# Optimization experiments

Hardware: AMD Instinct MI355X
Metric: run time of the kernel (lower is better)

The kernel has to match this reference:

```python
import jax, jax.numpy as jnp
import numpy as np

N, T, C = 2048, 32, 512          # stocks, lookback, channels (= embed_dim)
H, DH = 8, 64                    # heads, head_dim
NUM_IND = 64                     # number of industries
K1, S1, TS1 = 2, 2, 16           # conv scale 1
K2, S2, TS2 = 4, 4, 8            # conv scale 2
TC = T + TS1 + TS2               # concat_time_dim_for_triu = 56
EPS = 1e-5


def hardswish(x):
    return x * jnp.clip(x + 3.0, 0.0, 6.0) / 6.0


def _conv1d(x_nct, w, b, stride):
    # x_nct: [N, C, T], w: [C_out, C_in, K]
    y = jax.lax.conv_general_dilated(x_nct, w, (stride,), 'VALID',
                                     dimension_numbers=('NCH', 'OIH', 'NCH'))
    return y + b[None, :, None]


def _ln2d(y, g, b):
    # torch LayerNorm([ts, C]): normalize jointly over last two dims
    m = y.mean(axis=(-2, -1), keepdims=True)
    v = y.var(axis=(-2, -1), keepdims=True)
    return (y - m) / jnp.sqrt(v + EPS) * g + b


def _time_mixer(x, conv1_w, conv1_b, conv2_w, conv2_b,
                ln1_g, ln1_b, ln2_g, ln2_b,
                triu_w1, triu_b1, triu_w2, triu_b2):
    x_nct = x.transpose(0, 2, 1)                                   # [N, C, T]
    f1 = _ln2d(_conv1d(x_nct, conv1_w, conv1_b, S1).transpose(0, 2, 1), ln1_g, ln1_b)  # [N, TS1, C]
    f2 = _ln2d(_conv1d(x_nct, conv2_w, conv2_b, S2).transpose(0, 2, 1), ln2_g, ln2_b)  # [N, TS2, C]
    cat = jnp.concatenate([x, f1, f2], axis=1)                     # [N, TC, C]
    z = cat.transpose(0, 2, 1)                                     # [N, C, TC]
    # TriU: per-timestep Linear(i+1 -> 1) == lower-triangular matmul + bias
    h = jnp.einsum('nct,st->ncs', z, jnp.tril(triu_w1)) + triu_b1
    h = hardswish(h)
    h = jnp.einsum('nct,st->ncs', h, jnp.tril(triu_w2)) + triu_b2
    return h.transpose(0, 2, 1)                                    # [N, TC, C]


def _sparse_attn(tokens, industry_ids, wq, bq, wk, bk, wv, bv, wo, bo):
    # tokens: [N, C]; same-industry block-sparse attention (eval: no dropout)
    q = (tokens @ wq + bq).reshape(N, H, DH)
    k = (tokens @ wk + bk).reshape(N, H, DH)
    v = (tokens @ wv + bv).reshape(N, H, DH)
    scores = jnp.einsum('nhd,mhd->hnm', q, k) / jnp.sqrt(jnp.float32(DH))  # [H, N, N]
    mask = industry_ids[:, None] == industry_ids[None, :]                  # [N, N]
    scores = jnp.where(mask[None], scores, jnp.float32(-1e9))
    attn = jax.nn.softmax(scores, axis=-1)
    out = jnp.einsum('hnm,mhd->nhd', attn, v).reshape(N, C)
    return out @ wo + bo


def setup_inputs() -> dict:
    key = jax.random.key(0)
    ks = jax.random.split(key, 20)
    g = lambda k, s, sc=0.02: jax.random.normal(k, s, jnp.float32) * sc
    return {
        'x': jax.random.normal(ks[0], (N, T, C), jnp.float32),
        'industry_ids': jax.random.randint(ks[1], (N,), 0, NUM_IND),
        'conv1_w': g(ks[2], (C, C, K1)), 'conv1_b': jnp.zeros((C,), jnp.float32),
        'conv2_w': g(ks[3], (C, C, K2)), 'conv2_b': jnp.zeros((C,), jnp.float32),
        'ln1_g': jnp.ones((TS1, C), jnp.float32), 'ln1_b': jnp.zeros((TS1, C), jnp.float32),
        'ln2_g': jnp.ones((TS2, C), jnp.float32), 'ln2_b': jnp.zeros((TS2, C), jnp.float32),
        'triu_w1': g(ks[4], (TC, TC), 0.1), 'triu_b1': jnp.zeros((TC,), jnp.float32),
        'triu_w2': g(ks[5], (TC, TC), 0.1), 'triu_b2': jnp.zeros((TC,), jnp.float32),
        'wq': g(ks[6], (C, C)), 'bq': jnp.zeros((C,), jnp.float32),
        'wk': g(ks[7], (C, C)), 'bk': jnp.zeros((C,), jnp.float32),
        'wv': g(ks[8], (C, C)), 'bv': jnp.zeros((C,), jnp.float32),
        'wo': g(ks[9], (C, C)), 'bo': jnp.zeros((C,), jnp.float32),
        'wp': g(ks[10], (C, 1)), 'bp': jnp.zeros((1,), jnp.float32),
    }


def reference(x, industry_ids, conv1_w, conv1_b, conv2_w, conv2_b,
              ln1_g, ln1_b, ln2_g, ln2_b,
              triu_w1, triu_b1, triu_w2, triu_b2,
              wq, bq, wk, bk, wv, bv, wo, bo, wp, bp):
    mixed = _time_mixer(x, conv1_w, conv1_b, conv2_w, conv2_b,
                        ln1_g, ln1_b, ln2_g, ln2_b,
                        triu_w1, triu_b1, triu_w2, triu_b2)   # [N, TC, C]
    pooled = mixed.mean(axis=1)                                # [N, C]
    attn = _sparse_attn(pooled, industry_ids, wq, bq, wk, bk, wv, bv, wo, bo)
    h = pooled + attn                                          # residual
    return h @ wp + bp                                         # [N, 1]
```

## Files before the change

kernel.cpp:

```cpp
#include <hip/hip_runtime.h>

#define NST 2048

typedef __attribute__((ext_vector_type(8))) short bf16x8;
typedef __attribute__((ext_vector_type(4))) float f32x4;
typedef __attribute__((ext_vector_type(8))) unsigned short u16x8;

__device__ __forceinline__ float hswish(float x) {
  return x * fminf(fmaxf(x + 3.f, 0.f), 6.f) * (1.f / 6.f);
}

__device__ __forceinline__ unsigned short f2bf(float f) {
  unsigned int u = __float_as_uint(f);
  u += 0x7fffu + ((u >> 16) & 1u);
  return (unsigned short)(u >> 16);
}

__device__ __forceinline__ float bf2f(unsigned short b) {
  return __uint_as_float(((unsigned int)b) << 16);
}

__device__ __forceinline__ void gload16(const void* g, void* l) {
  __builtin_amdgcn_global_load_lds(
      (const __attribute__((address_space(1))) void*)g,
      (__attribute__((address_space(3))) void*)l, 16, 0, 0);
}

__global__ __launch_bounds__(256) void x_prep(const float* __restrict__ x,
                                              unsigned short* __restrict__ xbf,
                                              unsigned short* __restrict__ xT) {
  __shared__ unsigned short T[32 * 520];
  const int n = blockIdx.x;
  const int tid = threadIdx.x;
  const float* xn = x + (long)n * 16384;
  unsigned short* xbn = xbf + (long)n * 16384;

#pragma unroll
  for (int i = 0; i < 16; i++) {
    int id = tid + i * 256;
    int flat = id * 4;
    float4 v = *(const float4*)(xn + flat);
    short4 o;
    o.x = (short)f2bf(v.x); o.y = (short)f2bf(v.y);
    o.z = (short)f2bf(v.z); o.w = (short)f2bf(v.w);
    *(short4*)(xbn + flat) = o;
    int t = flat >> 9, c = flat & 511;
    *(short4*)&T[t * 520 + c] = o;
  }
  __syncthreads();

#pragma unroll
  for (int r = 0; r < 2; r++) {
    int c = tid + r * 256;
    unsigned short* dst = xT + ((long)n * 512 + c) * 32;
#pragma unroll
    for (int q = 0; q < 4; q++) {
      short4 o;
      o.x = (short)T[(q * 8 + 0) * 520 + c];
      o.y = (short)T[(q * 8 + 1) * 520 + c];
      o.z = (short)T[(q * 8 + 2) * 520 + c];
      o.w = (short)T[(q * 8 + 3) * 520 + c];
      short4 p;
      p.x = (short)T[(q * 8 + 4) * 520 + c];
      p.y = (short)T[(q * 8 + 5) * 520 + c];
      p.z = (short)T[(q * 8 + 6) * 520 + c];
      p.w = (short)T[(q * 8 + 7) * 520 + c];
      *(short4*)(dst + q * 8) = o;
      *(short4*)(dst + q * 8 + 4) = p;
    }
  }
}

__global__ __launch_bounds__(256) void conv_w_to_bt(const float* __restrict__ src,
                                                    unsigned short* __restrict__ dst,
                                                    int Kw, int rlshift) {
  int id = blockIdx.x * 256 + threadIdx.x;
  int co = id >> rlshift;
  int idx = id & ((1 << rlshift) - 1);
  int ci = idx & 511;
  int k = idx >> 9;
  dst[id] = f2bf(src[((co << 9) + ci) * Kw + k]);
}

__global__ __launch_bounds__(256) void qkv_w_to_bt(
    const float* __restrict__ wq, const float* __restrict__ wk,
    const float* __restrict__ wv, const float* __restrict__ bq,
    const float* __restrict__ bk, const float* __restrict__ bv,
    unsigned short* __restrict__ Bt, float* __restrict__ bias) {
  int id = blockIdx.x * 256 + threadIdx.x;
  int o = id >> 9, i = id & 511;
  int oc = o & 511;
  const float* w = (o < 512) ? wq : (o < 1024) ? wk : wv;
  Bt[id] = f2bf(w[(i << 9) + oc]);
  if (i == 0) bias[o] = (o < 512) ? bq[oc] : (o < 1024) ? bk[oc] : bv[oc];
}

__global__ __launch_bounds__(256) void triu_prep(
    const float* __restrict__ W1, const float* __restrict__ b1,
    const float* __restrict__ W2, const float* __restrict__ b2,
    unsigned short* __restrict__ W1bf, float* __restrict__ w2cp,
    float* __restrict__ b1p, float* __restrict__ b2s) {
  int tid = threadIdx.x;
#pragma unroll
  for (int i = 0; i < 16; i++) {
    int id = tid + i * 256;
    int s = id >> 6, t = id & 63;
    float v = (s < 56 && t < 56 && t <= s) ? W1[s * 56 + t] : 0.f;
    W1bf[id] = f2bf(v);
  }
  if (tid < 64) {
    float sum = 0.f;
    if (tid < 56)
      for (int r = tid; r < 56; r++) sum += W2[r * 56 + tid];
    w2cp[tid] = sum;
    b1p[tid] = (tid < 56) ? b1[tid] : 0.f;
  }
  if (tid == 0) {
    float b = 0.f;
    for (int s = 0; s < 56; s++) b += b2[s];
    b2s[0] = b;
  }
}

template <int MODE>
__global__ __launch_bounds__(256) void gemm_bt(
    const unsigned short* __restrict__ A, const unsigned short* __restrict__ Bt,
    float* __restrict__ C, unsigned short* __restrict__ fT,
    const float* __restrict__ bias, int K, int ldc) {
  __shared__ unsigned short As[128 * 64];
  __shared__ unsigned short Bs[128 * 64];
  const int tid = threadIdx.x;
  const int wid = tid >> 6;
  const int lane = tid & 63;
  const int r0 = blockIdx.x * 128;
  const int c0 = blockIdx.y * 128;
  const int wr = (wid >> 1) * 64;
  const int wc = (wid & 1) * 64;
  const int srow = lane >> 3;
  const int sslot = lane & 7;

  long aoffl[4], boffl[4];
  unsigned short* adst[4];
  unsigned short* bdst[4];
#pragma unroll
  for (int l = 0; l < 4; l++) {
    const int r = (wid * 4 + l) * 8 + srow;
    const int gr = r0 + r;
    long ao;
    if (MODE == 0)      ao = (long)(((gr >> 4) * 32) + ((gr & 15) << 1)) << 9;
    else if (MODE == 1) ao = (long)(((gr >> 3) * 32) + ((gr & 7) << 2)) << 9;
    else                ao = (long)gr * K;
    const int sw = (sslot ^ (r & 7)) << 3;
    aoffl[l] = ao + sw;
    boffl[l] = (long)(c0 + r) * K + sw;
    adst[l] = &As[(wid * 4 + l) * 8 * 64];
    bdst[l] = &Bs[(wid * 4 + l) * 8 * 64];
  }

  f32x4 acc[4][4];
#pragma unroll
  for (int m = 0; m < 4; m++)
#pragma unroll
    for (int n = 0; n < 4; n++) acc[m][n] = (f32x4){0.f, 0.f, 0.f, 0.f};

  const int fr = lane & 15;
  const int fq = lane >> 4;

  for (int kt = 0; kt < K; kt += 64) {
#pragma unroll
    for (int l = 0; l < 4; l++) {
      gload16(A + aoffl[l] + kt, adst[l]);
      gload16(Bt + boffl[l] + kt, bdst[l]);
    }
    __syncthreads();
#pragma unroll
    for (int ks = 0; ks < 2; ks++) {
      const int kq = ks * 4 + fq;
      bf16x8 af[4], bfr[4];
#pragma unroll
      for (int m = 0; m < 4; m++) {
        const int rr = wr + m * 16 + fr;
        af[m] = *(const bf16x8*)&As[rr * 64 + ((kq ^ (rr & 7)) << 3)];
      }
#pragma unroll
      for (int n = 0; n < 4; n++) {
        const int cc = wc + n * 16 + fr;
        bfr[n] = *(const bf16x8*)&Bs[cc * 64 + ((kq ^ (cc & 7)) << 3)];
      }
#pragma unroll
      for (int m = 0; m < 4; m++)
#pragma unroll
        for (int n = 0; n < 4; n++)
          acc[m][n] = __builtin_amdgcn_mfma_f32_16x16x32_bf16(
              af[m], bfr[n], acc[m][n], 0, 0, 0);
    }
    __syncthreads();
  }

  float bv[4];
#pragma unroll
  for (int n = 0; n < 4; n++) bv[n] = bias[c0 + wc + n * 16 + fr];

  if (MODE == 2) {
#pragma unroll
    for (int m = 0; m < 4; m++)
#pragma unroll
      for (int j = 0; j < 4; j++) {
        const int gr = r0 + wr + m * 16 + fq * 4 + j;
        float* cp = C + (long)gr * ldc + c0 + wc + fr;
#pragma unroll
        for (int n = 0; n < 4; n++) cp[n * 16] = acc[m][n][j] + bv[n];
      }
  } else {
#pragma unroll
    for (int m = 0; m < 4; m++) {
      const int gr = r0 + wr + m * 16 + fq * 4;
      int nst, e0;
      if (MODE == 0) { nst = gr >> 4; e0 = gr & 15; }
      else           { nst = gr >> 3; e0 = 16 + (gr & 7); }
#pragma unroll
      for (int n = 0; n < 4; n++) {
        const int cc = c0 + wc + n * 16 + fr;
        short4 o;
        o.x = (short)f2bf(acc[m][n][0] + bv[n]);
        o.y = (short)f2bf(acc[m][n][1] + bv[n]);
        o.z = (short)f2bf(acc[m][n][2] + bv[n]);
        o.w = (short)f2bf(acc[m][n][3] + bv[n]);
        *(short4*)(fT + ((long)(nst * 512 + cc) * 32 + e0)) = o;
      }
    }
  }
}

__global__ __launch_bounds__(256) void ln_fT(
    unsigned short* __restrict__ fT,
    const float* __restrict__ g1, const float* __restrict__ b1,
    const float* __restrict__ g2, const float* __restrict__ b2) {
  const int n = blockIdx.x;
  const int tid = threadIdx.x;
  const int w = tid >> 6, lane = tid & 63;
  __shared__ float red[4][4];
  unsigned short* base = fT + (long)n * 16384;

  u16x8 ch[8];
  float s1 = 0.f, q1 = 0.f, s2 = 0.f, q2 = 0.f;
#pragma unroll
  for (int i = 0; i < 8; i++) {
    int id = tid + i * 256;
    int qq = id & 3;
    if (qq != 3) {
      u16x8 v = *(const u16x8*)(base + (long)id * 8);
      ch[i] = v;
      float fs = 0.f, fq = 0.f;
#pragma unroll
      for (int j = 0; j < 8; j++) {
        float f = bf2f(v[j]);
        fs += f; fq += f * f;
      }
      if (qq < 2) { s1 += fs; q1 += fq; } else { s2 += fs; q2 += fq; }
    }
  }
  for (int d = 32; d; d >>= 1) {
    s1 += __shfl_down(s1, d); q1 += __shfl_down(q1, d);
    s2 += __shfl_down(s2, d); q2 += __shfl_down(q2, d);
  }
  if (lane == 0) { red[w][0] = s1; red[w][1] = q1; red[w][2] = s2; red[w][3] = q2; }
  __syncthreads();
  float S1 = red[0][0] + red[1][0] + red[2][0] + red[3][0];
  float Q1 = red[0][1] + red[1][1] + red[2][1] + red[3][1];
  float S2 = red[0][2] + red[1][2] + red[2][2] + red[3][2];
  float Q2 = red[0][3] + red[1][3] + red[2][3] + red[3][3];
  float m1 = S1 / 8192.f, v1 = Q1 / 8192.f - m1 * m1;
  float r1 = rsqrtf(v1 + 1e-5f);
  float m2 = S2 / 4096.f, v2 = Q2 / 4096.f - m2 * m2;
  float r2 = rsqrtf(v2 + 1e-5f);

#pragma unroll
  for (int i = 0; i < 8; i++) {
    int id = tid + i * 256;
    int qq = id & 3, c = id >> 2;
    u16x8 o;
    if (qq == 3) {
#pragma unroll
      for (int j = 0; j < 8; j++) o[j] = 0;
    } else {
      float m = (qq < 2) ? m1 : m2;
      float r = (qq < 2) ? r1 : r2;
#pragma unroll
      for (int j = 0; j < 8; j++) {
        float g, b;
        if (qq < 2) { int ts = qq * 8 + j; g = g1[ts * 512 + c]; b = b1[ts * 512 + c]; }
        else        { g = g2[j * 512 + c]; b = b2[j * 512 + c]; }
        float f = bf2f(ch[i][j]);
        o[j] = f2bf((f - m) * r * g + b);
      }
    }
    *(u16x8*)(base + (long)id * 8) = o;
  }
}

__global__ __launch_bounds__(512, 4) void triu_pool(
    const unsigned short* __restrict__ xT, const unsigned short* __restrict__ fT,
    const unsigned short* __restrict__ W1bf, const float* __restrict__ b1p,
    const float* __restrict__ w2cp, const float* __restrict__ b2s,
    float* __restrict__ pooled, unsigned short* __restrict__ pooledbf) {
  __shared__ unsigned short Zt[512 * 64];
  const int tid = threadIdx.x;
  const int wid = tid >> 6;
  const int lane = tid & 63;
  const int n = blockIdx.x;
  const int fr = lane & 15;
  const int fq = lane >> 4;

  const unsigned short* xTn = xT + (long)n * 16384;
  const unsigned short* fTn = fT + (long)n * 16384;

#pragma unroll
  for (int cb = 0; cb < 8; cb++) {
    const int cbase = wid * 64 + cb * 8;
    const int c = cbase + (lane >> 3);
    const int slot = lane & 7;
    const int slotp = slot ^ (c & 7);
    const unsigned short* src = (slotp < 4)
        ? (xTn + c * 32 + slotp * 8)
        : (fTn + c * 32 + (slotp - 4) * 8);
    gload16(src, &Zt[cbase * 64]);
  }
  __syncthreads();

  bf16x8 afr[4][2];
#pragma unroll
  for (int m = 0; m < 4; m++)
#pragma unroll
    for (int ks = 0; ks < 2; ks++)
      afr[m][ks] = *(const bf16x8*)(W1bf + (m * 16 + fr) * 64 + ks * 32 + fq * 8);

  f32x4 acc[4][4];
#pragma unroll
  for (int m = 0; m < 4; m++)
#pragma unroll
    for (int nn = 0; nn < 4; nn++) acc[m][nn] = (f32x4){0.f, 0.f, 0.f, 0.f};

#pragma unroll
  for (int nn = 0; nn < 4; nn++) {
    const int c = wid * 64 + nn * 16 + fr;
#pragma unroll
    for (int ks = 0; ks < 2; ks++) {
      const int slot = (ks * 4 + fq) ^ (c & 7);
      bf16x8 bfrag = *(const bf16x8*)&Zt[c * 64 + slot * 8];
#pragma unroll
      for (int m = 0; m < 4; m++)
        acc[m][nn] = __builtin_amdgcn_mfma_f32_16x16x32_bf16(
            afr[m][ks], bfrag, acc[m][nn], 0, 0, 0);
    }
  }

  float b1r[16], w2r[16];
#pragma unroll
  for (int m = 0; m < 4; m++)
#pragma unroll
    for (int j = 0; j < 4; j++) {
      int s = m * 16 + fq * 4 + j;
      b1r[m * 4 + j] = b1p[s];
      w2r[m * 4 + j] = w2cp[s];
    }
  const float b2sum = b2s[0];

#pragma unroll
  for (int nn = 0; nn < 4; nn++) {
    float cs = 0.f;
#pragma unroll
    for (int m = 0; m < 4; m++)
#pragma unroll
      for (int j = 0; j < 4; j++)
        cs = fmaf(hswish(acc[m][nn][j] + b1r[m * 4 + j]), w2r[m * 4 + j], cs);
    cs += __shfl_xor(cs, 16);
    cs += __shfl_xor(cs, 32);
    if (fq == 0) {
      const int c = wid * 64 + nn * 16 + fr;
      float pv = (cs + b2sum) * (1.f / 56.f);
      pooled[(long)n * 512 + c] = pv;
      pooledbf[(long)n * 512 + c] = f2bf(pv);
    }
  }
}

__global__ void binzero(int* counts, int* cursor) {
  int i = threadIdx.x;
  if (i < 64) { counts[i] = 0; cursor[i] = 0; }
}
__global__ void bincount(const int* __restrict__ ids, int* counts) {
  int n = blockIdx.x * 256 + threadIdx.x;
  if (n < NST) atomicAdd(&counts[ids[n]], 1);
}
__global__ void binscan(const int* __restrict__ counts, int* offs) {
  int lane = threadIdx.x;
  int incl = counts[lane];
  for (int d = 1; d < 64; d <<= 1) {
    int u = __shfl_up(incl, d);
    if (lane >= d) incl += u;
  }
  offs[lane + 1] = incl;
  if (lane == 0) offs[0] = 0;
}
__global__ void binscatter(const int* __restrict__ ids, const int* __restrict__ offs,
                           int* cursor, int* perm) {
  int n = blockIdx.x * 256 + threadIdx.x;
  if (n < NST) {
    int g = ids[n];
    int pos = offs[g] + atomicAdd(&cursor[g], 1);
    perm[pos] = n;
  }
}

__global__ __launch_bounds__(256) void attn_kernel(
    const float* __restrict__ qkv, const int* __restrict__ offs,
    const int* __restrict__ perm, float* __restrict__ attnv) {
  const int g = blockIdx.x, h = blockIdx.y;
  const int off = offs[g];
  const int S = offs[g + 1] - off;
  const int tid = threadIdx.x;
  const int w = tid >> 6, lane = tid & 63;

  __shared__ float Ks[128 * 66];
  __shared__ float Vs[128 * 64];
  __shared__ float Ps[4][128];
  __shared__ float Qw[4][64];

  if (S <= 128) {
    for (int idx = tid; idx < S * 16; idx += 256) {
      const int row = idx >> 4, q4 = (idx & 15) * 4;
      const int mj = perm[off + row];
      const float* base = qkv + (long)mj * 1536 + h * 64 + q4;
      float4 kv = *(const float4*)(base + 512);
      float4 vv = *(const float4*)(base + 1024);
      float* kr = &Ks[row * 66 + q4];
      kr[0] = kv.x; kr[1] = kv.y; kr[2] = kv.z; kr[3] = kv.w;
      *(float4*)&Vs[row * 64 + q4] = vv;
    }
    __syncthreads();

    for (int i = w; i < S; i += 4) {
      const int mi = perm[off + i];
      const float qd = qkv[(long)mi * 1536 + h * 64 + lane];
      Qw[w][lane] = qd;

      float sc0 = -1e30f, sc1 = -1e30f;
      {
        const int j = lane;
        if (j < S) {
          float a = 0.f;
          const float* kr = &Ks[j * 66];
#pragma unroll
          for (int t = 0; t < 32; t++) {
            float2 k2 = *(const float2*)(kr + 2 * t);
            float2 q2 = *(const float2*)&Qw[w][2 * t];
            a = fmaf(q2.x, k2.x, a);
            a = fmaf(q2.y, k2.y, a);
          }
          sc0 = a * 0.125f;
        }
      }
      if (S > 64) {
        const int j = 64 + lane;
        if (j < S) {
          float a = 0.f;
          const float* kr = &Ks[j * 66];
#pragma unroll
          for (int t = 0; t < 32; t++) {
            float2 k2 = *(const float2*)(kr + 2 * t);
            float2 q2 = *(const float2*)&Qw[w][2 * t];
            a = fmaf(q2.x, k2.x, a);
            a = fmaf(q2.y, k2.y, a);
          }
          sc1 = a * 0.125f;
        }
      }
      float m = fmaxf(sc0, sc1);
      for (int d = 32; d; d >>= 1) m = fmaxf(m, __shfl_xor(m, d));
      float p0 = (lane < S) ? __expf(sc0 - m) : 0.f;
      float p1 = (64 + lane < S) ? __expf(sc1 - m) : 0.f;
      float l = p0 + p1;
      for (int d = 32; d; d >>= 1) l += __shfl_xor(l, d);
      Ps[w][lane] = p0;
      Ps[w][64 + lane] = p1;

      float o = 0.f;
      for (int j = 0; j < S; j++)
        o = fmaf(Ps[w][j], Vs[j * 64 + lane], o);
      attnv[(long)mi * 512 + h * 64 + lane] = o / l;
    }
  } else {
    __shared__ float pbuf[4][64];
    __shared__ int jbuf[4][64];
    for (int i = w; i < S; i += 4) {
      const int mi = perm[off + i];
      const float* qp = qkv + (long)mi * 1536 + h * 64;
      float m_run = -1e30f, l_run = 0.f, o_d = 0.f;
      for (int jb = 0; jb < S; jb += 64) {
        int jc = min(64, S - jb);
        int mj = (lane < jc) ? perm[off + jb + lane] : 0;
        float sc = -1e30f;
        if (lane < jc) {
          const float* kp = qkv + (long)mj * 1536 + 512 + h * 64;
          float a = 0.f;
#pragma unroll
          for (int d4 = 0; d4 < 16; d4++) {
            float4 qv = *(const float4*)(qp + d4 * 4);
            float4 kv = *(const float4*)(kp + d4 * 4);
            a += qv.x * kv.x + qv.y * kv.y + qv.z * kv.z + qv.w * kv.w;
          }
          sc = a * 0.125f;
        }
        float cm = sc;
        for (int d = 32; d; d >>= 1) cm = fmaxf(cm, __shfl_xor(cm, d));
        float m_new = fmaxf(m_run, cm);
        float resc = __expf(m_run - m_new);
        float p = (lane < jc) ? __expf(sc - m_new) : 0.f;
        float cs = p;
        for (int d = 32; d; d >>= 1) cs += __shfl_xor(cs, d);
        l_run = l_run * resc + cs;
        pbuf[w][lane] = p;
        jbuf[w][lane] = mj;
        float onew = o_d * resc;
        for (int j = 0; j < jc; j++)
          onew = fmaf(pbuf[w][j], qkv[(long)jbuf[w][j] * 1536 + 1024 + h * 64 + lane], onew);
        o_d = onew;
        m_run = m_new;
      }
      attnv[(long)mi * 512 + h * 64 + lane] = o_d / l_run;
    }
  }
}

__global__ void wowp_kernel(const float* __restrict__ wo, const float* __restrict__ wp,
                            const float* __restrict__ bo, const float* __restrict__ bp,
                            float* wowp, float* constbuf) {
  int w = threadIdx.x >> 6, lane = threadIdx.x & 63;
  int gw = blockIdx.x * 4 + w;
  for (int row = gw; row < 512; row += 32) {
    float partial = 0.f;
    for (int e = lane; e < 512; e += 64) partial += wo[(long)row * 512 + e] * wp[e];
    for (int d = 32; d; d >>= 1) partial += __shfl_xor(partial, d);
    if (lane == 0) wowp[row] = partial;
  }
  if (blockIdx.x == 0 && w == 0) {
    float partial = 0.f;
    for (int e = lane; e < 512; e += 64) partial += bo[e] * wp[e];
    for (int d = 32; d; d >>= 1) partial += __shfl_xor(partial, d);
    if (lane == 0) constbuf[0] = partial + bp[0];
  }
}

__global__ void final_kernel(const float* __restrict__ pooled,
                             const float* __restrict__ attnv,
                             const float* __restrict__ wp,
                             const float* __restrict__ wowp,
                             const float* __restrict__ constbuf,
                             float* __restrict__ out) {
  int w = threadIdx.x >> 6, lane = threadIdx.x & 63;
  int row = blockIdx.x * 4 + w;
  float partial = 0.f;
#pragma unroll
  for (int e8 = 0; e8 < 8; e8++) {
    int e = lane + e8 * 64;
    partial += pooled[(long)row * 512 + e] * wp[e] + attnv[(long)row * 512 + e] * wowp[e];
  }
  for (int d = 32; d; d >>= 1) partial += __shfl_xor(partial, d);
  if (lane == 0) out[row] = partial + constbuf[0];
}

extern "C" void kernel_launch(void* const* d_in, const int* in_sizes, int n_in,
                              void* d_out, int out_size, void* d_ws, size_t ws_size,
                              hipStream_t stream) {
  const float* x   = (const float*)d_in[0];
  const int*   ids = (const int*)d_in[1];
  const float* w1  = (const float*)d_in[2];
  const float* cb1 = (const float*)d_in[3];
  const float* w2  = (const float*)d_in[4];
  const float* cb2 = (const float*)d_in[5];
  const float* g1  = (const float*)d_in[6];
  const float* lb1 = (const float*)d_in[7];
  const float* g2  = (const float*)d_in[8];
  const float* lb2 = (const float*)d_in[9];
  const float* tw1 = (const float*)d_in[10];
  const float* tb1 = (const float*)d_in[11];
  const float* tw2 = (const float*)d_in[12];
  const float* tb2 = (const float*)d_in[13];
  const float* wq  = (const float*)d_in[14];
  const float* bq  = (const float*)d_in[15];
  const float* wk  = (const float*)d_in[16];
  const float* bk  = (const float*)d_in[17];
  const float* wv  = (const float*)d_in[18];
  const float* bv  = (const float*)d_in[19];
  const float* wo  = (const float*)d_in[20];
  const float* bo  = (const float*)d_in[21];
  const float* wp  = (const float*)d_in[22];
  const float* bp  = (const float*)d_in[23];
  float* out = (float*)d_out;

  char* ws = (char*)d_ws;
  size_t off = 0;
  auto alloc = [&](size_t bytes) {
    void* p = ws + off;
    off += (bytes + 255) & ~(size_t)255;
    return p;
  };
  unsigned short* xbf  = (unsigned short*)alloc((size_t)NST * 32 * 512 * 2);
  unsigned short* xT   = (unsigned short*)alloc((size_t)NST * 512 * 32 * 2);
  unsigned short* fT   = (unsigned short*)alloc((size_t)NST * 512 * 32 * 2);
  unsigned short* B1b  = (unsigned short*)alloc((size_t)512 * 1024 * 2);
  unsigned short* B2b  = (unsigned short*)alloc((size_t)512 * 2048 * 2);
  unsigned short* Bqkv = (unsigned short*)alloc((size_t)1536 * 512 * 2);
  float* bqkv   = (float*)alloc(1536 * 4);
  unsigned short* W1bf = (unsigned short*)alloc(64 * 64 * 2);
  float* w2cp   = (float*)alloc(64 * 4);
  float* b1p    = (float*)alloc(64 * 4);
  float* b2s    = (float*)alloc(4);
  float* pooled = (float*)alloc((size_t)NST * 512 * 4);
  unsigned short* pooledbf = (unsigned short*)alloc((size_t)NST * 512 * 2);
  float* qkvb   = (float*)alloc((size_t)NST * 1536 * 4);
  float* attnv  = (float*)alloc((size_t)NST * 512 * 4);
  float* wowp   = (float*)alloc(512 * 4);
  float* cbuf   = (float*)alloc(4);
  int* counts   = (int*)alloc(64 * 4);
  int* cursor   = (int*)alloc(64 * 4);
  int* offs     = (int*)alloc(65 * 4);
  int* perm     = (int*)alloc(NST * 4);

  x_prep<<<NST, 256, 0, stream>>>(x, xbf, xT);
  conv_w_to_bt<<<dim3(512 * 1024 / 256), 256, 0, stream>>>(w1, B1b, 2, 10);
  conv_w_to_bt<<<dim3(512 * 2048 / 256), 256, 0, stream>>>(w2, B2b, 4, 11);
  qkv_w_to_bt<<<dim3(1536 * 512 / 256), 256, 0, stream>>>(wq, wk, wv, bq, bk, bv, Bqkv, bqkv);
  triu_prep<<<1, 256, 0, stream>>>(tw1, tb1, tw2, tb2, W1bf, w2cp, b1p, b2s);
  binzero<<<1, 64, 0, stream>>>(counts, cursor);
  bincount<<<8, 256, 0, stream>>>(ids, counts);
  binscan<<<1, 64, 0, stream>>>(counts, offs);
  binscatter<<<8, 256, 0, stream>>>(ids, offs, cursor, perm);
  wowp_kernel<<<8, 256, 0, stream>>>(wo, wp, bo, bp, wowp, cbuf);

  gemm_bt<0><<<dim3(256, 4), 256, 0, stream>>>(xbf, B1b, nullptr, fT, cb1, 1024, 0);
  gemm_bt<1><<<dim3(128, 4), 256, 0, stream>>>(xbf, B2b, nullptr, fT, cb2, 2048, 0);
  ln_fT<<<NST, 256, 0, stream>>>(fT, g1, lb1, g2, lb2);
  triu_pool<<<NST, 512, 0, stream>>>(xT, fT, W1bf, b1p, w2cp, b2s, pooled, pooledbf);

  gemm_bt<2><<<dim3(16, 12), 256, 0, stream>>>(pooledbf, Bqkv, qkvb, nullptr, bqkv, 512, 1536);

  attn_kernel<<<dim3(64, 8), 256, 0, stream>>>(qkvb, offs, perm, attnv);
  final_kernel<<<512, 256, 0, stream>>>(pooled, attnv, wp, wowp, cbuf, out);
}
```

Measured before the change: 606.8 us.

## Merge prep kernels, fuse conv GEMMs, fold LayerNorm into triu_pool

Combines the weight-conversion, triu-prep and wo·wp kernels into a single launch, and collapses the four binning kernels into one block that uses shared-memory atomics. The two conv GEMMs become one grid, and the separate LayerNorm pass over fT is moved into triu_pool, which now normalises the data already staged in LDS. x_prep's transpose now uses 16-byte stores with a changed LDS padding. These changes remove several launches and one full read/write round trip of fT, at the cost of extra LDS work and a sync inside triu_pool.

```diff
diff --git a/kernel.cpp b/kernel.cpp
--- a/kernel.cpp
+++ b/kernel.cpp
@@ -29,7 +29,7 @@
 __global__ __launch_bounds__(256) void x_prep(const float* __restrict__ x,
                                               unsigned short* __restrict__ xbf,
                                               unsigned short* __restrict__ xT) {
-  __shared__ unsigned short T[32 * 520];
+  __shared__ unsigned short T[32 * 524];
   const int n = blockIdx.x;
   const int tid = threadIdx.x;
   const float* xn = x + (long)n * 16384;
@@ -45,88 +45,219 @@
     o.z = (short)f2bf(v.z); o.w = (short)f2bf(v.w);
     *(short4*)(xbn + flat) = o;
     int t = flat >> 9, c = flat & 511;
-    *(short4*)&T[t * 520 + c] = o;
+    *(short4*)&T[t * 524 + c] = o;
   }
   __syncthreads();
 
-#pragma unroll
-  for (int r = 0; r < 2; r++) {
-    int c = tid + r * 256;
-    unsigned short* dst = xT + ((long)n * 512 + c) * 32;
-#pragma unroll
-    for (int q = 0; q < 4; q++) {
-      short4 o;
-      o.x = (short)T[(q * 8 + 0) * 520 + c];
-      o.y = (short)T[(q * 8 + 1) * 520 + c];
-      o.z = (short)T[(q * 8 + 2) * 520 + c];
-      o.w = (short)T[(q * 8 + 3) * 520 + c];
-      short4 p;
-      p.x = (short)T[(q * 8 + 4) * 520 + c];
-      p.y = (short)T[(q * 8 + 5) * 520 + c];
-      p.z = (short)T[(q * 8 + 6) * 520 + c];
-      p.w = (short)T[(q * 8 + 7) * 520 + c];
-      *(short4*)(dst + q * 8) = o;
-      *(short4*)(dst + q * 8 + 4) = p;
-    }
-  }
-}
-
-__global__ __launch_bounds__(256) void conv_w_to_bt(const float* __restrict__ src,
-                                                    unsigned short* __restrict__ dst,
-                                                    int Kw, int rlshift) {
-  int id = blockIdx.x * 256 + threadIdx.x;
-  int co = id >> rlshift;
-  int idx = id & ((1 << rlshift) - 1);
-  int ci = idx & 511;
-  int k = idx >> 9;
-  dst[id] = f2bf(src[((co << 9) + ci) * Kw + k]);
-}
-
-__global__ __launch_bounds__(256) void qkv_w_to_bt(
+  const int q = tid & 3;
+  const int csub = tid >> 2;
+#pragma unroll
+  for (int rr = 0; rr < 8; rr++) {
+    int c = rr * 64 + csub;
+    u16x8 o;
+#pragma unroll
+    for (int j = 0; j < 8; j++) o[j] = T[(q * 8 + j) * 524 + c];
+    *(u16x8*)(xT + (long)n * 16384 + c * 32 + q * 8) = o;
+  }
+}
+
+__global__ __launch_bounds__(256) void weights_prep(
+    const float* __restrict__ w1, const float* __restrict__ w2,
     const float* __restrict__ wq, const float* __restrict__ wk,
     const float* __restrict__ wv, const float* __restrict__ bq,
     const float* __restrict__ bk, const float* __restrict__ bv,
-    unsigned short* __restrict__ Bt, float* __restrict__ bias) {
-  int id = blockIdx.x * 256 + threadIdx.x;
-  int o = id >> 9, i = id & 511;
-  int oc = o & 511;
-  const float* w = (o < 512) ? wq : (o < 1024) ? wk : wv;
-  Bt[id] = f2bf(w[(i << 9) + oc]);
-  if (i == 0) bias[o] = (o < 512) ? bq[oc] : (o < 1024) ? bk[oc] : bv[oc];
-}
-
-__global__ __launch_bounds__(256) void triu_prep(
-    const float* __restrict__ W1, const float* __restrict__ b1,
-    const float* __restrict__ W2, const float* __restrict__ b2,
+    const float* __restrict__ tw1, const float* __restrict__ tb1,
+    const float* __restrict__ tw2, const float* __restrict__ tb2,
+    const float* __restrict__ wo, const float* __restrict__ wp,
+    const float* __restrict__ bo, const float* __restrict__ bp,
+    unsigned short* __restrict__ B1b, unsigned short* __restrict__ B2b,
+    unsigned short* __restrict__ Bqkv, float* __restrict__ bqkv,
     unsigned short* __restrict__ W1bf, float* __restrict__ w2cp,
-    float* __restrict__ b1p, float* __restrict__ b2s) {
-  int tid = threadIdx.x;
-#pragma unroll
-  for (int i = 0; i < 16; i++) {
-    int id = tid + i * 256;
-    int s = id >> 6, t = id & 63;
-    float v = (s < 56 && t < 56 && t <= s) ? W1[s * 56 + t] : 0.f;
-    W1bf[id] = f2bf(v);
-  }
+    float* __restrict__ b1p, float* __restrict__ b2s,
+    float* __restrict__ wowp, float* __restrict__ cbuf) {
+  const int b = blockIdx.x, tid = threadIdx.x;
+  if (b < 2048) {
+    int id = b * 256 + tid;
+    int co = id >> 10, idx = id & 1023, ci = idx & 511, k = idx >> 9;
+    B1b[id] = f2bf(w1[((co << 9) + ci) * 2 + k]);
+  } else if (b < 6144) {
+    int id = (b - 2048) * 256 + tid;
+    int co = id >> 11, idx = id & 2047, ci = idx & 511, k = idx >> 9;
+    B2b[id] = f2bf(w2[((co << 9) + ci) * 4 + k]);
+  } else if (b < 9216) {
+    int id = (b - 6144) * 256 + tid;
+    int o = id >> 9, i = id & 511, oc = o & 511;
+    const float* w = (o < 512) ? wq : (o < 1024) ? wk : wv;
+    Bqkv[id] = f2bf(w[(i << 9) + oc]);
+    if (i == 0) bqkv[o] = (o < 512) ? bq[oc] : (o < 1024) ? bk[oc] : bv[oc];
+  } else if (b == 9216) {
+#pragma unroll
+    for (int i = 0; i < 16; i++) {
+      int id = tid + i * 256;
+      int s = id >> 6, t = id & 63;
+      float v = (s < 56 && t < 56 && t <= s) ? tw1[s * 56 + t] : 0.f;
+      W1bf[id] = f2bf(v);
+    }
+    if (tid < 64) {
+      float sum = 0.f;
+      if (tid < 56)
+        for (int r = tid; r < 56; r++) sum += tw2[r * 56 + tid];
+      w2cp[tid] = sum;
+      b1p[tid] = (tid < 56) ? tb1[tid] : 0.f;
+    }
+    if (tid == 0) {
+      float bb = 0.f;
+      for (int s = 0; s < 56; s++) bb += tb2[s];
+      b2s[0] = bb;
+    }
+  } else {
+    int w = tid >> 6, lane = tid & 63;
+    int gw = (b - 9217) * 4 + w;
+    for (int row = gw; row < 512; row += 32) {
+      float partial = 0.f;
+      for (int e = lane; e < 512; e += 64) partial += wo[(long)row * 512 + e] * wp[e];
+      for (int d = 32; d; d >>= 1) partial += __shfl_xor(partial, d);
+      if (lane == 0) wowp[row] = partial;
+    }
+    if (b == 9217 && w == 0) {
+      float partial = 0.f;
+      for (int e = lane; e < 512; e += 64) partial += bo[e] * wp[e];
+      for (int d = 32; d; d >>= 1) partial += __shfl_xor(partial, d);
+      if (lane == 0) cbuf[0] = partial + bp[0];
+    }
+  }
+}
+
+__global__ __launch_bounds__(1024) void binning(const int* __restrict__ ids,
+                                                int* __restrict__ offs_g,
+                                                int* __restrict__ perm) {
+  __shared__ int cnt[64], cur[64], offs_s[65];
+  const int tid = threadIdx.x;
+  if (tid < 64) { cnt[tid] = 0; cur[tid] = 0; }
+  __syncthreads();
+  for (int n = tid; n < NST; n += 1024) atomicAdd(&cnt[ids[n]], 1);
+  __syncthreads();
   if (tid < 64) {
-    float sum = 0.f;
-    if (tid < 56)
-      for (int r = tid; r < 56; r++) sum += W2[r * 56 + tid];
-    w2cp[tid] = sum;
-    b1p[tid] = (tid < 56) ? b1[tid] : 0.f;
-  }
-  if (tid == 0) {
-    float b = 0.f;
-    for (int s = 0; s < 56; s++) b += b2[s];
-    b2s[0] = b;
-  }
-}
-
-template <int MODE>
-__global__ __launch_bounds__(256) void gemm_bt(
+    int incl = cnt[tid];
+    for (int d = 1; d < 64; d <<= 1) {
+      int u = __shfl_up(incl, d);
+      if (tid >= d) incl += u;
+    }
+    offs_s[tid + 1] = incl;
+    offs_g[tid + 1] = incl;
+    if (tid == 0) { offs_s[0] = 0; offs_g[0] = 0; }
+  }
+  __syncthreads();
+  for (int n = tid; n < NST; n += 1024) {
+    int g = ids[n];
+    perm[offs_s[g] + atomicAdd(&cur[g], 1)] = n;
+  }
+}
+
+__global__ __launch_bounds__(256) void gemm_conv(
+    const unsigned short* __restrict__ A, const unsigned short* __restrict__ B1,
+    const unsigned short* __restrict__ B2, unsigned short* __restrict__ fT,
+    const float* __restrict__ cb1, const float* __restrict__ cb2) {
+  __shared__ unsigned short As[128 * 64];
+  __shared__ unsigned short Bs[128 * 64];
+  const int tid = threadIdx.x;
+  const int wid = tid >> 6;
+  const int lane = tid & 63;
+  const bool isc1 = blockIdx.x < 256;
+  const int bx = isc1 ? blockIdx.x : blockIdx.x - 256;
+  const unsigned short* Bt = isc1 ? B1 : B2;
+  const float* bias = isc1 ? cb1 : cb2;
+  const int K = isc1 ? 1024 : 2048;
+  const int r0 = bx * 128;
+  const int c0 = blockIdx.y * 128;
+  const int wr = (wid >> 1) * 64;
+  const int wc = (wid & 1) * 64;
+  const int srow = lane >> 3;
+  const int sslot = lane & 7;
+
+  long aoffl[4], boffl[4];
+  unsigned short* adst[4];
+  unsigned short* bdst[4];
+#pragma unroll
+  for (int l = 0; l < 4; l++) {
+    const int r = (wid * 4 + l) * 8 + srow;
+    const int gr = r0 + r;
+    long ao;
+    if (isc1) ao = (long)(((gr >> 4) * 32) + ((gr & 15) << 1)) << 9;
+    else      ao = (long)(((gr >> 3) * 32) + ((gr & 7) << 2)) << 9;
+    const int sw = (sslot ^ (r & 7)) << 3;
+    aoffl[l] = ao + sw;
+    boffl[l] = (long)(c0 + r) * K + sw;
+    adst[l] = &As[(wid * 4 + l) * 8 * 64];
+    bdst[l] = &Bs[(wid * 4 + l) * 8 * 64];
+  }
+
+  f32x4 acc[4][4];
+#pragma unroll
+  for (int m = 0; m < 4; m++)
+#pragma unroll
+    for (int n = 0; n < 4; n++) acc[m][n] = (f32x4){0.f, 0.f, 0.f, 0.f};
+
+  const int fr = lane & 15;
+  const int fq = lane >> 4;
+
+  for (int kt = 0; kt < K; kt += 64) {
+#pragma unroll
+    for (int l = 0; l < 4; l++) {
+      gload16(A + aoffl[l] + kt, adst[l]);
+      gload16(Bt + boffl[l] + kt, bdst[l]);
+    }
+    __syncthreads();
+#pragma unroll
+    for (int ks = 0; ks < 2; ks++) {
+      const int kq = ks * 4 + fq;
+      bf16x8 af[4], bfr[4];
+#pragma unroll
+      for (int m = 0; m < 4; m++) {
+        const int rr = wr + m * 16 + fr;
+        af[m] = *(const bf16x8*)&As[rr * 64 + ((kq ^ (rr & 7)) << 3)];
+      }
+#pragma unroll
+      for (int n = 0; n < 4; n++) {
+        const int cc = wc + n * 16 + fr;
+        bfr[n] = *(const bf16x8*)&Bs[cc * 64 + ((kq ^ (cc & 7)) << 3)];
+      }
+#pragma unroll
+      for (int m = 0; m < 4; m++)
+#pragma unroll
+        for (int n = 0; n < 4; n++)
+          acc[m][n] = __builtin_amdgcn_mfma_f32_16x16x32_bf16(
+              af[m], bfr[n], acc[m][n], 0, 0, 0);
+    }
+    __syncthreads();
+  }
+
+  float bv[4];
+#pragma unroll
+  for (int n = 0; n < 4; n++) bv[n] = bias[c0 + wc + n * 16 + fr];
+
+#pragma unroll
+  for (int m = 0; m < 4; m++) {
+    const int gr = r0 + wr + m * 16 + fq * 4;
+    int nst, e0;
+    if (isc1) { nst = gr >> 4; e0 = gr & 15; }
+    else      { nst = gr >> 3; e0 = 16 + (gr & 7); }
+#pragma unroll
+    for (int n = 0; n < 4; n++) {
+      const int cc = c0 + wc + n * 16 + fr;
+      short4 o;
+      o.x = (short)f2bf(acc[m][n][0] + bv[n]);
+      o.y = (short)f2bf(acc[m][n][1] + bv[n]);
+      o.z = (short)f2bf(acc[m][n][2] + bv[n]);
+      o.w = (short)f2bf(acc[m][n][3] + bv[n]);
+      *(short4*)(fT + ((long)(nst * 512 + cc) * 32 + e0)) = o;
+    }
+  }
+}
+
+__global__ __launch_bounds__(256) void gemm_qkv(
     const unsigned short* __restrict__ A, const unsigned short* __restrict__ Bt,
-    float* __restrict__ C, unsigned short* __restrict__ fT,
-    const float* __restrict__ bias, int K, int ldc) {
+    float* __restrict__ C, const float* __restrict__ bias, int K, int ldc) {
   __shared__ unsigned short As[128 * 64];
   __shared__ unsigned short Bs[128 * 64];
   const int tid = threadIdx.x;
@@ -146,12 +277,8 @@
   for (int l = 0; l < 4; l++) {
     const int r = (wid * 4 + l) * 8 + srow;
     const int gr = r0 + r;
-    long ao;
-    if (MODE == 0)      ao = (long)(((gr >> 4) * 32) + ((gr & 15) << 1)) << 9;
-    else if (MODE == 1) ao = (long)(((gr >> 3) * 32) + ((gr & 7) << 2)) << 9;
-    else                ao = (long)gr * K;
     const int sw = (sslot ^ (r & 7)) << 3;
-    aoffl[l] = ao + sw;
+    aoffl[l] = (long)gr * K + sw;
     boffl[l] = (long)(c0 + r) * K + sw;
     adst[l] = &As[(wid * 4 + l) * 8 * 64];
     bdst[l] = &Bs[(wid * 4 + l) * 8 * 64];
@@ -201,110 +328,26 @@
 #pragma unroll
   for (int n = 0; n < 4; n++) bv[n] = bias[c0 + wc + n * 16 + fr];
 
-  if (MODE == 2) {
-#pragma unroll
-    for (int m = 0; m < 4; m++)
-#pragma unroll
-      for (int j = 0; j < 4; j++) {
-        const int gr = r0 + wr + m * 16 + fq * 4 + j;
-        float* cp = C + (long)gr * ldc + c0 + wc + fr;
-#pragma unroll
-        for (int n = 0; n < 4; n++) cp[n * 16] = acc[m][n][j] + bv[n];
-      }
-  } else {
-#pragma unroll
-    for (int m = 0; m < 4; m++) {
-      const int gr = r0 + wr + m * 16 + fq * 4;
-      int nst, e0;
-      if (MODE == 0) { nst = gr >> 4; e0 = gr & 15; }
-      else           { nst = gr >> 3; e0 = 16 + (gr & 7); }
-#pragma unroll
-      for (int n = 0; n < 4; n++) {
-        const int cc = c0 + wc + n * 16 + fr;
-        short4 o;
-        o.x = (short)f2bf(acc[m][n][0] + bv[n]);
-        o.y = (short)f2bf(acc[m][n][1] + bv[n]);
-        o.z = (short)f2bf(acc[m][n][2] + bv[n]);
-        o.w = (short)f2bf(acc[m][n][3] + bv[n]);
-        *(short4*)(fT + ((long)(nst * 512 + cc) * 32 + e0)) = o;
-      }
-    }
-  }
-}
-
-__global__ __launch_bounds__(256) void ln_fT(
-    unsigned short* __restrict__ fT,
-    const float* __restrict__ g1, const float* __restrict__ b1,
-    const float* __restrict__ g2, const float* __restrict__ b2) {
-  const int n = blockIdx.x;
-  const int tid = threadIdx.x;
-  const int w = tid >> 6, lane = tid & 63;
-  __shared__ float red[4][4];
-  unsigned short* base = fT + (long)n * 16384;
-
-  u16x8 ch[8];
-  float s1 = 0.f, q1 = 0.f, s2 = 0.f, q2 = 0.f;
-#pragma unroll
-  for (int i = 0; i < 8; i++) {
-    int id = tid + i * 256;
-    int qq = id & 3;
-    if (qq != 3) {
-      u16x8 v = *(const u16x8*)(base + (long)id * 8);
-      ch[i] = v;
-      float fs = 0.f, fq = 0.f;
-#pragma unroll
-      for (int j = 0; j < 8; j++) {
-        float f = bf2f(v[j]);
-        fs += f; fq += f * f;
-      }
-      if (qq < 2) { s1 += fs; q1 += fq; } else { s2 += fs; q2 += fq; }
-    }
-  }
-  for (int d = 32; d; d >>= 1) {
-    s1 += __shfl_down(s1, d); q1 += __shfl_down(q1, d);
-    s2 += __shfl_down(s2, d); q2 += __shfl_down(q2, d);
-  }
-  if (lane == 0) { red[w][0] = s1; red[w][1] = q1; red[w][2] = s2; red[w][3] = q2; }
-  __syncthreads();
-  float S1 = red[0][0] + red[1][0] + red[2][0] + red[3][0];
-  float Q1 = red[0][1] + red[1][1] + red[2][1] + red[3][1];
-  float S2 = red[0][2] + red[1][2] + red[2][2] + red[3][2];
-  float Q2 = red[0][3] + red[1][3] + red[2][3] + red[3][3];
-  float m1 = S1 / 8192.f, v1 = Q1 / 8192.f - m1 * m1;
-  float r1 = rsqrtf(v1 + 1e-5f);
-  float m2 = S2 / 4096.f, v2 = Q2 / 4096.f - m2 * m2;
-  float r2 = rsqrtf(v2 + 1e-5f);
-
-#pragma unroll
-  for (int i = 0; i < 8; i++) {
-    int id = tid + i * 256;
-    int qq = id & 3, c = id >> 2;
-    u16x8 o;
-    if (qq == 3) {
-#pragma unroll
-      for (int j = 0; j < 8; j++) o[j] = 0;
-    } else {
-      float m = (qq < 2) ? m1 : m2;
-      float r = (qq < 2) ? r1 : r2;
-#pragma unroll
-      for (int j = 0; j < 8; j++) {
-        float g, b;
-        if (qq < 2) { int ts = qq * 8 + j; g = g1[ts * 512 + c]; b = b1[ts * 512 + c]; }
-        else        { g = g2[j * 512 + c]; b = b2[j * 512 + c]; }
-        float f = bf2f(ch[i][j]);
-        o[j] = f2bf((f - m) * r * g + b);
-      }
-    }
-    *(u16x8*)(base + (long)id * 8) = o;
-  }
+#pragma unroll
+  for (int m = 0; m < 4; m++)
+#pragma unroll
+    for (int j = 0; j < 4; j++) {
+      const int gr = r0 + wr + m * 16 + fq * 4 + j;
+      float* cp = C + (long)gr * ldc + c0 + wc + fr;
+#pragma unroll
+      for (int n = 0; n < 4; n++) cp[n * 16] = acc[m][n][j] + bv[n];
+    }
 }
 
 __global__ __launch_bounds__(512, 4) void triu_pool(
     const unsigned short* __restrict__ xT, const unsigned short* __restrict__ fT,
     const unsigned short* __restrict__ W1bf, const float* __restrict__ b1p,
     const float* __restrict__ w2cp, const float* __restrict__ b2s,
+    const float* __restrict__ g1, const float* __restrict__ lb1,
+    const float* __restrict__ g2, const float* __restrict__ lb2,
     float* __restrict__ pooled, unsigned short* __restrict__ pooledbf) {
   __shared__ unsigned short Zt[512 * 64];
+  __shared__ float red[8][4];
   const int tid = threadIdx.x;
   const int wid = tid >> 6;
   const int lane = tid & 63;
@@ -328,6 +371,50 @@
   }
   __syncthreads();
 
+  const int c = tid;
+  const int cx = c & 7;
+  bf16x8 f1a = *(const bf16x8*)&Zt[c * 64 + ((4 ^ cx) << 3)];
+  bf16x8 f1b = *(const bf16x8*)&Zt[c * 64 + ((5 ^ cx) << 3)];
+  bf16x8 f2a = *(const bf16x8*)&Zt[c * 64 + ((6 ^ cx) << 3)];
+  float s1 = 0.f, q1 = 0.f, s2 = 0.f, q2 = 0.f;
+#pragma unroll
+  for (int j = 0; j < 8; j++) {
+    float a = bf2f((unsigned short)f1a[j]);
+    float b = bf2f((unsigned short)f1b[j]);
+    float d = bf2f((unsigned short)f2a[j]);
+    s1 += a + b; q1 += a * a + b * b;
+    s2 += d;     q2 += d * d;
+  }
+  for (int d = 32; d; d >>= 1) {
+    s1 += __shfl_xor(s1, d); q1 += __shfl_xor(q1, d);
+    s2 += __shfl_xor(s2, d); q2 += __shfl_xor(q2, d);
+  }
+  if (lane == 0) { red[wid][0] = s1; red[wid][1] = q1; red[wid][2] = s2; red[wid][3] = q2; }
+  __syncthreads();
+  float S1 = 0.f, Q1 = 0.f, S2 = 0.f, Q2 = 0.f;
+#pragma unroll
+  for (int wv = 0; wv < 8; wv++) {
+    S1 += red[wv][0]; Q1 += red[wv][1]; S2 += red[wv][2]; Q2 += red[wv][3];
+  }
+  const float m1 = S1 / 8192.f;
+  const float r1 = rsqrtf(Q1 / 8192.f - m1 * m1 + 1e-5f);
+  const float m2 = S2 / 4096.f;
+  const float r2 = rsqrtf(Q2 / 4096.f - m2 * m2 + 1e-5f);
+
+  u16x8 o1a, o1b, o2a, zz;
+#pragma unroll
+  for (int j = 0; j < 8; j++) {
+    o1a[j] = f2bf((bf2f((unsigned short)f1a[j]) - m1) * r1 * g1[j * 512 + c] + lb1[j * 512 + c]);
+    o1b[j] = f2bf((bf2f((unsigned short)f1b[j]) - m1) * r1 * g1[(8 + j) * 512 + c] + lb1[(8 + j) * 512 + c]);
+    o2a[j] = f2bf((bf2f((unsigned short)f2a[j]) - m2) * r2 * g2[j * 512 + c] + lb2[j * 512 + c]);
+    zz[j] = 0;
+  }
+  *(u16x8*)&Zt[c * 64 + ((4 ^ cx) << 3)] = o1a;
+  *(u16x8*)&Zt[c * 64 + ((5 ^ cx) << 3)] = o1b;
+  *(u16x8*)&Zt[c * 64 + ((6 ^ cx) << 3)] = o2a;
+  *(u16x8*)&Zt[c * 64 + ((7 ^ cx) << 3)] = zz;
+  __syncthreads();
+
   bf16x8 afr[4][2];
 #pragma unroll
   for (int m = 0; m < 4; m++)
@@ -343,11 +430,11 @@
 
 #pragma unroll
   for (int nn = 0; nn < 4; nn++) {
-    const int c = wid * 64 + nn * 16 + fr;
+    const int cc = wid * 64 + nn * 16 + fr;
 #pragma unroll
     for (int ks = 0; ks < 2; ks++) {
-      const int slot = (ks * 4 + fq) ^ (c & 7);
-      bf16x8 bfrag = *(const bf16x8*)&Zt[c * 64 + slot * 8];
+      const int slot = (ks * 4 + fq) ^ (cc & 7);
+      bf16x8 bfrag = *(const bf16x8*)&Zt[cc * 64 + slot * 8];
 #pragma unroll
       for (int m = 0; m < 4; m++)
         acc[m][nn] = __builtin_amdgcn_mfma_f32_16x16x32_bf16(
@@ -377,39 +464,11 @@
     cs += __shfl_xor(cs, 16);
     cs += __shfl_xor(cs, 32);
     if (fq == 0) {
-      const int c = wid * 64 + nn * 16 + fr;
+      const int cc = wid * 64 + nn * 16 + fr;
       float pv = (cs + b2sum) * (1.f / 56.f);
-      pooled[(long)n * 512 + c] = pv;
-      pooledbf[(long)n * 512 + c] = f2bf(pv);
-    }
-  }
-}
-
-__global__ void binzero(int* counts, int* cursor) {
-  int i = threadIdx.x;
-  if (i < 64) { counts[i] = 0; cursor[i] = 0; }
-}
-__global__ void bincount(const int* __restrict__ ids, int* counts) {
-  int n = blockIdx.x * 256 + threadIdx.x;
-  if (n < NST) atomicAdd(&counts[ids[n]], 1);
-}
-__global__ void binscan(const int* __restrict__ counts, int* offs) {
-  int lane = threadIdx.x;
-  int incl = counts[lane];
-  for (int d = 1; d < 64; d <<= 1) {
-    int u = __shfl_up(incl, d);
-    if (lane >= d) incl += u;
-  }
-  offs[lane + 1] = incl;
-  if (lane == 0) offs[0] = 0;
-}
-__global__ void binscatter(const int* __restrict__ ids, const int* __restrict__ offs,
-                           int* cursor, int* perm) {
-  int n = blockIdx.x * 256 + threadIdx.x;
-  if (n < NST) {
-    int g = ids[n];
-    int pos = offs[g] + atomicAdd(&cursor[g], 1);
-    perm[pos] = n;
+      pooled[(long)n * 512 + cc] = pv;
+      pooledbf[(long)n * 512 + cc] = f2bf(pv);
+    }
   }
 }
 
@@ -530,25 +589,6 @@
       }
       attnv[(long)mi * 512 + h * 64 + lane] = o_d / l_run;
     }
-  }
-}
-
-__global__ void wowp_kernel(const float* __restrict__ wo, const float* __restrict__ wp,
-                            const float* __restrict__ bo, const float* __restrict__ bp,
-                            float* wowp, float* constbuf) {
-  int w = threadIdx.x >> 6, lane = threadIdx.x & 63;
-  int gw = blockIdx.x * 4 + w;
-  for (int row = gw; row < 512; row += 32) {
-    float partial = 0.f;
-    for (int e = lane; e < 512; e += 64) partial += wo[(long)row * 512 + e] * wp[e];
-    for (int d = 32; d; d >>= 1) partial += __shfl_xor(partial, d);
-    if (lane == 0) wowp[row] = partial;
-  }
-  if (blockIdx.x == 0 && w == 0) {
-    float partial = 0.f;
-    for (int e = lane; e < 512; e += 64) partial += bo[e] * wp[e];
-    for (int d = 32; d; d >>= 1) partial += __shfl_xor(partial, d);
-    if (lane == 0) constbuf[0] = partial + bp[0];
   }
 }
 
@@ -623,28 +663,22 @@
   float* attnv  = (float*)alloc((size_t)NST * 512 * 4);
   float* wowp   = (float*)alloc(512 * 4);
   float* cbuf   = (float*)alloc(4);
-  int* counts   = (int*)alloc(64 * 4);
-  int* cursor   = (int*)alloc(64 * 4);
   int* offs     = (int*)alloc(65 * 4);
   int* perm     = (int*)alloc(NST * 4);
 
+  weights_prep<<<9225, 256, 0, stream>>>(w1, w2, wq, wk, wv, bq, bk, bv,
+                                         tw1, tb1, tw2, tb2, wo, wp, bo, bp,
+                                         B1b, B2b, Bqkv, bqkv, W1bf, w2cp, b1p, b2s,
+                                         wowp, cbuf);
+  binning<<<1, 1024, 0, stream>>>(ids, offs, perm);
   x_prep<<<NST, 256, 0, stream>>>(x, xbf, xT);
-  conv_w_to_bt<<<dim3(512 * 1024 / 256), 256, 0, stream>>>(w1, B1b, 2, 10);
-  conv_w_to_bt<<<dim3(512 * 2048 / 256), 256, 0, stream>>>(w2, B2b, 4, 11);
-  qkv_w_to_bt<<<dim3(1536 * 512 / 256), 256, 0, stream>>>(wq, wk, wv, bq, bk, bv, Bqkv, bqkv);
-  triu_prep<<<1, 256, 0, stream>>>(tw1, tb1, tw2, tb2, W1bf, w2cp, b1p, b2s);
-  binzero<<<1, 64, 0, stream>>>(counts, cursor);
-  bincount<<<8, 256, 0, stream>>>(ids, counts);
-  binscan<<<1, 64, 0, stream>>>(counts, offs);
-  binscatter<<<8, 256, 0, stream>>>(ids, offs, cursor, perm);
-  wowp_kernel<<<8, 256, 0, stream>>>(wo, wp, bo, bp, wowp, cbuf);
-
-  gemm_bt<0><<<dim3(256, 4), 256, 0, stream>>>(xbf, B1b, nullptr, fT, cb1, 1024, 0);
-  gemm_bt<1><<<dim3(128, 4), 256, 0, stream>>>(xbf, B2b, nullptr, fT, cb2, 2048, 0);
-  ln_fT<<<NST, 256, 0, stream>>>(fT, g1, lb1, g2, lb2);
-  triu_pool<<<NST, 512, 0, stream>>>(xT, fT, W1bf, b1p, w2cp, b2s, pooled, pooledbf);
-
-  gemm_bt<2><<<dim3(16, 12), 256, 0, stream>>>(pooledbf, Bqkv, qkvb, nullptr, bqkv, 512, 1536);
+
+  gemm_conv<<<dim3(384, 4), 256, 0, stream>>>(xbf, B1b, B2b, fT, cb1, cb2);
+
+  triu_pool<<<NST, 512, 0, stream>>>(xT, fT, W1bf, b1p, w2cp, b2s,
+                                     g1, lb1, g2, lb2, pooled, pooledbf);
+
+  gemm_qkv<<<dim3(16, 12), 256, 0, stream>>>(pooledbf, Bqkv, qkvb, bqkv, 512, 1536);
 
   attn_kernel<<<dim3(64, 8), 256, 0, stream>>>(qkvb, offs, perm, attnv);
   final_kernel<<<512, 256, 0, stream>>>(pooled, attnv, wp, wowp, cbuf, out);
```

New measurement: 559.7 us. 1.08x faster.
